# Optimization experiments

Hardware: AMD Instinct MI355X
Metric: run time of the kernel (lower is better)

Reference implementation:

```python
import jax, jax.numpy as jnp
import numpy as np

SEQ, B, IN, H = 2048, 4096, 1, 32


def setup_inputs() -> dict:
    key = jax.random.key(0)
    ks = jax.random.split(key, 8)
    s_ih = 1.0 / np.sqrt(H)  # torch nn.RNN init scale
    return {
        "x": jax.random.normal(ks[0], (SEQ, B, IN), dtype=jnp.float32),
        "hidden": jnp.zeros((1, B, H), dtype=jnp.float32),
        "W_ih": jax.random.uniform(ks[1], (H, IN), jnp.float32, -s_ih, s_ih),
        "b_ih": jax.random.uniform(ks[2], (H,), jnp.float32, -s_ih, s_ih),
        "W_hh": jax.random.uniform(ks[3], (H, H), jnp.float32, -s_ih, s_ih),
        "b_hh": jax.random.uniform(ks[4], (H,), jnp.float32, -s_ih, s_ih),
        "W_fc": jax.random.uniform(ks[5], (IN, H), jnp.float32, -s_ih, s_ih),
        "b_fc": jax.random.uniform(ks[6], (IN,), jnp.float32, -s_ih, s_ih),
    }


def reference(x, hidden, W_ih, b_ih, W_hh, b_hh, W_fc, b_fc):
    # Elman RNN: h_t = tanh(x_t W_ih^T + b_ih + h_{t-1} W_hh^T + b_hh)
    # Precompute the input projection for all timesteps in one GEMM.
    x_proj = jnp.einsum('sbi,hi->sbh', x, W_ih) + b_ih + b_hh  # (SEQ, B, H)
    h0 = hidden[0]  # (B, H), single layer

    def step(h, xp_t):
        h_new = jnp.tanh(xp_t + h @ W_hh.T)
        return h_new, h_new

    _, outputs = jax.lax.scan(step, h0, x_proj)  # outputs: (SEQ, B, H)
    # Trailing Linear: (SEQ, B, H) -> (SEQ, B, IN)
    return jnp.einsum('sbh,oh->sbo', outputs, W_fc) + b_fc
```

## Files before the change

### kernel.cpp

```cpp
#include <hip/hip_runtime.h>

#define SEQ   2048
#define BATCH 4096
#define HD    32

__device__ __forceinline__ float exp2_fast(float a) {
#if __has_builtin(__builtin_amdgcn_exp2f)
    return __builtin_amdgcn_exp2f(a);
#else
    return exp2f(a);
#endif
}

__device__ __forceinline__ float rcp_fast(float a) {
#if __has_builtin(__builtin_amdgcn_rcpf)
    return __builtin_amdgcn_rcpf(a);
#else
    return 1.0f / a;
#endif
}

__device__ __forceinline__ float fast_tanh(float v) {
    float ax = fabsf(v);
    float e  = exp2_fast(ax * -2.8853900817779268f);
    float r  = (1.0f - e) * rcp_fast(1.0f + e);
    return copysignf(r, v);
}

template <int CTRL>
__device__ __forceinline__ float dpp_mov0(float v) {
    return __int_as_float(
        __builtin_amdgcn_update_dpp(0, __float_as_int(v), CTRL, 0xF, 0xF, false));
}

__global__ __launch_bounds__(256) void rnn_elman_kernel(
    const float* __restrict__ x, const float* __restrict__ hidden,
    const float* __restrict__ W_ih, const float* __restrict__ b_ih,
    const float* __restrict__ W_hh, const float* __restrict__ b_hh,
    const float* __restrict__ W_fc, const float* __restrict__ b_fc,
    float* __restrict__ out)
{
    __shared__ float sh[16 * 36];

    const int tid = threadIdx.x;
    const int s   = tid & 15;
    const int eb  = tid >> 4;
    const int e   = blockIdx.x * 16 + eb;
    const int r0  = 2 * s;
    const int r1  = 2 * s + 1;

    float4 w0[8], w1[8];
    {
        const float4* W0 = reinterpret_cast<const float4*>(W_hh + r0 * HD);
        const float4* W1 = reinterpret_cast<const float4*>(W_hh + r1 * HD);
        #pragma unroll
        for (int k = 0; k < 8; ++k) { w0[k] = W0[k]; w1[k] = W1[k]; }
    }
    const float wih0  = W_ih[r0], wih1 = W_ih[r1];
    const float bias0 = b_ih[r0] + b_hh[r0];
    const float bias1 = b_ih[r1] + b_hh[r1];
    const float wfc0  = W_fc[r0], wfc1 = W_fc[r1];
    const float bfc   = b_fc[0];

    float* slot = sh + eb * 36;
    reinterpret_cast<float2*>(slot)[s] =
        make_float2(hidden[e * HD + r0], hidden[e * HD + r1]);
    __builtin_amdgcn_wave_barrier();

    float4 hb[8];
    #pragma unroll
    for (int k = 0; k < 8; ++k) hb[k] = reinterpret_cast<const float4*>(slot)[k];

    float xq0 = x[0 * BATCH + e];
    float xq1 = x[1 * BATCH + e];
    float xq2 = x[2 * BATCH + e];
    float xq3 = x[3 * BATCH + e];

    #pragma unroll 4
    for (int t = 0; t < SEQ; ++t) {
        const float xv = xq0;
        xq0 = xq1; xq1 = xq2; xq2 = xq3;
        {
            int tt = t + 4; tt = tt < SEQ - 1 ? tt : SEQ - 1;
            xq3 = x[tt * BATCH + e];
        }

        float a0a = fmaf(xv, wih0, bias0);
        float a1a = fmaf(xv, wih1, bias1);
        float a0b = 0.f, a0c = 0.f, a0d = 0.f;
        float a1b = 0.f, a1c = 0.f, a1d = 0.f;
        #pragma unroll
        for (int k = 0; k < 8; ++k) {
            const float4 h4 = hb[k];
            const float4 ww = w0[k];
            const float4 vv = w1[k];
            a0a = fmaf(ww.x, h4.x, a0a);
            a0b = fmaf(ww.y, h4.y, a0b);
            a0c = fmaf(ww.z, h4.z, a0c);
            a0d = fmaf(ww.w, h4.w, a0d);
            a1a = fmaf(vv.x, h4.x, a1a);
            a1b = fmaf(vv.y, h4.y, a1b);
            a1c = fmaf(vv.z, h4.z, a1c);
            a1d = fmaf(vv.w, h4.w, a1d);
        }
        const float z0 = (a0a + a0b) + (a0c + a0d);
        const float z1 = (a1a + a1b) + (a1c + a1d);

        const float h0 = fast_tanh(z0);
        const float h1 = fast_tanh(z1);

        reinterpret_cast<float2*>(slot)[s] = make_float2(h0, h1);
        __builtin_amdgcn_wave_barrier();
        #pragma unroll
        for (int k = 0; k < 8; ++k) hb[k] = reinterpret_cast<const float4*>(slot)[k];

        float p = fmaf(h0, wfc0, h1 * wfc1);
        p += dpp_mov0<0x111>(p);
        p += dpp_mov0<0x112>(p);
        p += dpp_mov0<0x114>(p);
        p += dpp_mov0<0x118>(p);
        if (s == 15) out[t * BATCH + e] = p + bfc;
    }
}

extern "C" void kernel_launch(void* const* d_in, const int* in_sizes, int n_in,
                              void* d_out, int out_size, void* d_ws, size_t ws_size,
                              hipStream_t stream) {
    const float* x    = (const float*)d_in[0];
    const float* hid  = (const float*)d_in[1];
    const float* W_ih = (const float*)d_in[2];
    const float* b_ih = (const float*)d_in[3];
    const float* W_hh = (const float*)d_in[4];
    const float* b_hh = (const float*)d_in[5];
    const float* W_fc = (const float*)d_in[6];
    const float* b_fc = (const float*)d_in[7];
    float* out = (float*)d_out;

    dim3 grid(BATCH / 16);
    dim3 block(256);
    rnn_elman_kernel<<<grid, block, 0, stream>>>(x, hid, W_ih, b_ih, W_hh, b_hh,
                                                 W_fc, b_fc, out);
}
```

Before: 594.4 us.

## Split each batch element's hidden matvec across 32 lanes with swizzle exchange

Each batch element now gets 32 lanes instead of 16. Every lane computes half of the K-dimension for its own row and for its partner's row. The partial sums are exchanged with a ds_swizzle xor-16, so each lane produces one hidden unit per step. This halves the per-lane FMA chain and register footprint on the serial recurrence and doubles the thread count, with launch bounds raised to allow more waves. In exchange it adds a cross-lane swizzle and an extra reduction stage on the critical path every timestep.

```diff
diff --git a/kernel.cpp b/kernel.cpp
--- a/kernel.cpp
+++ b/kernel.cpp
@@ -33,43 +33,49 @@
         __builtin_amdgcn_update_dpp(0, __float_as_int(v), CTRL, 0xF, 0xF, false));
 }
 
-__global__ __launch_bounds__(256) void rnn_elman_kernel(
+__device__ __forceinline__ float swz_xor16(float v) {
+    return __int_as_float(__builtin_amdgcn_ds_swizzle(__float_as_int(v), 0x401F));
+}
+
+__global__ __launch_bounds__(256, 2) void rnn_elman_kernel(
     const float* __restrict__ x, const float* __restrict__ hidden,
     const float* __restrict__ W_ih, const float* __restrict__ b_ih,
     const float* __restrict__ W_hh, const float* __restrict__ b_hh,
     const float* __restrict__ W_fc, const float* __restrict__ b_fc,
     float* __restrict__ out)
 {
-    __shared__ float sh[16 * 36];
+    __shared__ float sh[8 * 36];
 
-    const int tid = threadIdx.x;
-    const int s   = tid & 15;
-    const int eb  = tid >> 4;
-    const int e   = blockIdx.x * 16 + eb;
-    const int r0  = 2 * s;
-    const int r1  = 2 * s + 1;
+    const int tid   = threadIdx.x;
+    const int s     = tid & 31;
+    const int half  = s >> 4;
+    const int q     = s & 15;
+    const int eb    = tid >> 5;
+    const int e     = blockIdx.x * 8 + eb;
+    const int r_own = 2 * q + half;
+    const int r_oth = 2 * q + 1 - half;
 
-    float4 w0[8], w1[8];
+    float4 wo[4], wn[4];
     {
-        const float4* W0 = reinterpret_cast<const float4*>(W_hh + r0 * HD);
-        const float4* W1 = reinterpret_cast<const float4*>(W_hh + r1 * HD);
+        const float4* WO = reinterpret_cast<const float4*>(W_hh + r_own * HD + half * 16);
+        const float4* WN = reinterpret_cast<const float4*>(W_hh + r_oth * HD + half * 16);
         #pragma unroll
-        for (int k = 0; k < 8; ++k) { w0[k] = W0[k]; w1[k] = W1[k]; }
+        for (int k = 0; k < 4; ++k) { wo[k] = WO[k]; wn[k] = WN[k]; }
     }
-    const float wih0  = W_ih[r0], wih1 = W_ih[r1];
-    const float bias0 = b_ih[r0] + b_hh[r0];
-    const float bias1 = b_ih[r1] + b_hh[r1];
-    const float wfc0  = W_fc[r0], wfc1 = W_fc[r1];
-    const float bfc   = b_fc[0];
+    const float wih  = W_ih[r_own];
+    const float bias = b_ih[r_own] + b_hh[r_own];
+    const float wfc  = W_fc[r_own];
+    const float bfc  = b_fc[0];
 
     float* slot = sh + eb * 36;
-    reinterpret_cast<float2*>(slot)[s] =
-        make_float2(hidden[e * HD + r0], hidden[e * HD + r1]);
+    const float4* rd = reinterpret_cast<const float4*>(slot + half * 16);
+
+    slot[r_own] = hidden[e * HD + r_own];
     __builtin_amdgcn_wave_barrier();
 
-    float4 hb[8];
+    float4 hb[4];
     #pragma unroll
-    for (int k = 0; k < 8; ++k) hb[k] = reinterpret_cast<const float4*>(slot)[k];
+    for (int k = 0; k < 4; ++k) hb[k] = rd[k];
 
     float xq0 = x[0 * BATCH + e];
     float xq1 = x[1 * BATCH + e];
@@ -85,41 +91,51 @@
             xq3 = x[tt * BATCH + e];
         }
 
-        float a0a = fmaf(xv, wih0, bias0);
-        float a1a = fmaf(xv, wih1, bias1);
-        float a0b = 0.f, a0c = 0.f, a0d = 0.f;
-        float a1b = 0.f, a1c = 0.f, a1d = 0.f;
+        float a0 = fmaf(xv, wih, bias);
+        float a1 = 0.f;
+        float b0 = 0.f, b1 = 0.f;
         #pragma unroll
-        for (int k = 0; k < 8; ++k) {
+        for (int k = 0; k < 2; ++k) {
             const float4 h4 = hb[k];
-            const float4 ww = w0[k];
-            const float4 vv = w1[k];
-            a0a = fmaf(ww.x, h4.x, a0a);
-            a0b = fmaf(ww.y, h4.y, a0b);
-            a0c = fmaf(ww.z, h4.z, a0c);
-            a0d = fmaf(ww.w, h4.w, a0d);
-            a1a = fmaf(vv.x, h4.x, a1a);
-            a1b = fmaf(vv.y, h4.y, a1b);
-            a1c = fmaf(vv.z, h4.z, a1c);
-            a1d = fmaf(vv.w, h4.w, a1d);
+            const float4 h5 = hb[k + 2];
+            const float4 u  = wo[k];
+            const float4 v  = wo[k + 2];
+            const float4 m  = wn[k];
+            const float4 n  = wn[k + 2];
+            a0 = fmaf(u.x, h4.x, a0);
+            a0 = fmaf(u.y, h4.y, a0);
+            a0 = fmaf(u.z, h4.z, a0);
+            a0 = fmaf(u.w, h4.w, a0);
+            a1 = fmaf(v.x, h5.x, a1);
+            a1 = fmaf(v.y, h5.y, a1);
+            a1 = fmaf(v.z, h5.z, a1);
+            a1 = fmaf(v.w, h5.w, a1);
+            b0 = fmaf(m.x, h4.x, b0);
+            b0 = fmaf(m.y, h4.y, b0);
+            b0 = fmaf(m.z, h4.z, b0);
+            b0 = fmaf(m.w, h4.w, b0);
+            b1 = fmaf(n.x, h5.x, b1);
+            b1 = fmaf(n.y, h5.y, b1);
+            b1 = fmaf(n.z, h5.z, b1);
+            b1 = fmaf(n.w, h5.w, b1);
         }
-        const float z0 = (a0a + a0b) + (a0c + a0d);
-        const float z1 = (a1a + a1b) + (a1c + a1d);
+        const float own = a0 + a1;
+        const float oth = b0 + b1;
+        const float z   = own + swz_xor16(oth);
+        const float h   = fast_tanh(z);
 
-        const float h0 = fast_tanh(z0);
-        const float h1 = fast_tanh(z1);
-
-        reinterpret_cast<float2*>(slot)[s] = make_float2(h0, h1);
+        slot[r_own] = h;
         __builtin_amdgcn_wave_barrier();
         #pragma unroll
-        for (int k = 0; k < 8; ++k) hb[k] = reinterpret_cast<const float4*>(slot)[k];
+        for (int k = 0; k < 4; ++k) hb[k] = rd[k];
 
-        float p = fmaf(h0, wfc0, h1 * wfc1);
+        float p = h * wfc;
         p += dpp_mov0<0x111>(p);
         p += dpp_mov0<0x112>(p);
         p += dpp_mov0<0x114>(p);
         p += dpp_mov0<0x118>(p);
-        if (s == 15) out[t * BATCH + e] = p + bfc;
+        p += dpp_mov0<0x142>(p);
+        if (s == 31) out[t * BATCH + e] = p + bfc;
     }
 }
 
@@ -136,7 +152,7 @@
     const float* b_fc = (const float*)d_in[7];
     float* out = (float*)d_out;
 
-    dim3 grid(BATCH / 16);
+    dim3 grid(BATCH / 8);
     dim3 block(256);
     rnn_elman_kernel<<<grid, block, 0, stream>>>(x, hid, W_ih, b_ih, W_hh, b_hh,
                                                  W_fc, b_fc, out);
```

Result: slower. 616.2 us (+3.7%).

## Split hidden dot products across 32 lanes per batch element with DPP reductions

Applied to the files above, without the earlier changes.

Each batch element now gets a full 32 lanes instead of 16. Each lane covers a quarter of the K dimension for four rows, so the recurrent matvec per lane shrinks from 64 to 32 FMAs. Per-step LDS reads drop from eight float4 loads to two. The partial sums are combined with quad-permute DPP moves, and the output projection uses DPP mirrors plus a ds_swizzle xor-16. The grid doubles to 512 blocks and launch bounds request two blocks per CU, trading more waves and extra cross-lane reduction work for a shorter serial dependency chain per timestep.

```diff
diff --git a/kernel.cpp b/kernel.cpp
--- a/kernel.cpp
+++ b/kernel.cpp
@@ -28,98 +28,108 @@
 }
 
 template <int CTRL>
-__device__ __forceinline__ float dpp_mov0(float v) {
+__device__ __forceinline__ float dpp_x(float v) {
     return __int_as_float(
         __builtin_amdgcn_update_dpp(0, __float_as_int(v), CTRL, 0xF, 0xF, false));
 }
 
-__global__ __launch_bounds__(256) void rnn_elman_kernel(
+__device__ __forceinline__ float swz_xor16(float v) {
+    return __int_as_float(__builtin_amdgcn_ds_swizzle(__float_as_int(v), 0x401F));
+}
+
+__global__ __launch_bounds__(256, 2) void rnn_elman_kernel(
     const float* __restrict__ x, const float* __restrict__ hidden,
     const float* __restrict__ W_ih, const float* __restrict__ b_ih,
     const float* __restrict__ W_hh, const float* __restrict__ b_hh,
     const float* __restrict__ W_fc, const float* __restrict__ b_fc,
     float* __restrict__ out)
 {
-    __shared__ float sh[16 * 36];
+    __shared__ float sh[8 * 36];
 
     const int tid = threadIdx.x;
-    const int s   = tid & 15;
-    const int eb  = tid >> 4;
-    const int e   = blockIdx.x * 16 + eb;
-    const int r0  = 2 * s;
-    const int r1  = 2 * s + 1;
+    const int i   = tid & 31;
+    const int ks  = i & 3;
+    const int eb  = tid >> 5;
+    const int e   = blockIdx.x * 8 + eb;
 
-    float4 w0[8], w1[8];
+    float w0[8], w1[8], w2[8], w3[8];
     {
-        const float4* W0 = reinterpret_cast<const float4*>(W_hh + r0 * HD);
-        const float4* W1 = reinterpret_cast<const float4*>(W_hh + r1 * HD);
+        const int rbase = i & ~3;
+        const float* R0 = W_hh + (rbase | (ks ^ 0)) * HD + ks * 8;
+        const float* R1 = W_hh + (rbase | (ks ^ 1)) * HD + ks * 8;
+        const float* R2 = W_hh + (rbase | (ks ^ 2)) * HD + ks * 8;
+        const float* R3 = W_hh + (rbase | (ks ^ 3)) * HD + ks * 8;
         #pragma unroll
-        for (int k = 0; k < 8; ++k) { w0[k] = W0[k]; w1[k] = W1[k]; }
+        for (int m = 0; m < 8; ++m) {
+            w0[m] = R0[m]; w1[m] = R1[m]; w2[m] = R2[m]; w3[m] = R3[m];
+        }
     }
-    const float wih0  = W_ih[r0], wih1 = W_ih[r1];
-    const float bias0 = b_ih[r0] + b_hh[r0];
-    const float bias1 = b_ih[r1] + b_hh[r1];
-    const float wfc0  = W_fc[r0], wfc1 = W_fc[r1];
-    const float bfc   = b_fc[0];
+    const float wih  = W_ih[i];
+    const float bias = b_ih[i] + b_hh[i];
+    const float wfc  = W_fc[i];
+    const float bfc  = b_fc[0];
 
     float* slot = sh + eb * 36;
-    reinterpret_cast<float2*>(slot)[s] =
-        make_float2(hidden[e * HD + r0], hidden[e * HD + r1]);
+    const float4* rd = reinterpret_cast<const float4*>(slot + ks * 8);
+
+    slot[i] = hidden[e * HD + i];
     __builtin_amdgcn_wave_barrier();
+    float4 hb0 = rd[0], hb1 = rd[1];
 
-    float4 hb[8];
-    #pragma unroll
-    for (int k = 0; k < 8; ++k) hb[k] = reinterpret_cast<const float4*>(slot)[k];
-
-    float xq0 = x[0 * BATCH + e];
-    float xq1 = x[1 * BATCH + e];
-    float xq2 = x[2 * BATCH + e];
-    float xq3 = x[3 * BATCH + e];
+    float xq0 = x[(size_t)0 * BATCH + e];
+    float xq1 = x[(size_t)1 * BATCH + e];
+    float xq2 = x[(size_t)2 * BATCH + e];
+    float xq3 = x[(size_t)3 * BATCH + e];
 
     #pragma unroll 4
     for (int t = 0; t < SEQ; ++t) {
         const float xv = xq0;
         xq0 = xq1; xq1 = xq2; xq2 = xq3;
         {
-            int tt = t + 4; tt = tt < SEQ - 1 ? tt : SEQ - 1;
-            xq3 = x[tt * BATCH + e];
+            int tt = t + 4; tt = tt < SEQ ? tt : SEQ - 1;
+            const float* xr = x + (size_t)tt * BATCH;
+            xq3 = xr[e];
         }
 
-        float a0a = fmaf(xv, wih0, bias0);
-        float a1a = fmaf(xv, wih1, bias1);
-        float a0b = 0.f, a0c = 0.f, a0d = 0.f;
-        float a1b = 0.f, a1c = 0.f, a1d = 0.f;
-        #pragma unroll
-        for (int k = 0; k < 8; ++k) {
-            const float4 h4 = hb[k];
-            const float4 ww = w0[k];
-            const float4 vv = w1[k];
-            a0a = fmaf(ww.x, h4.x, a0a);
-            a0b = fmaf(ww.y, h4.y, a0b);
-            a0c = fmaf(ww.z, h4.z, a0c);
-            a0d = fmaf(ww.w, h4.w, a0d);
-            a1a = fmaf(vv.x, h4.x, a1a);
-            a1b = fmaf(vv.y, h4.y, a1b);
-            a1c = fmaf(vv.z, h4.z, a1c);
-            a1d = fmaf(vv.w, h4.w, a1d);
+        float p0 = fmaf(xv, wih, bias);
+        float p1 = 0.f, p2 = 0.f, p3 = 0.f;
+        {
+            const float* hv0 = reinterpret_cast<const float*>(&hb0);
+            const float* hv1 = reinterpret_cast<const float*>(&hb1);
+            #pragma unroll
+            for (int m = 0; m < 4; ++m) {
+                const float ha = hv0[m];
+                const float hc = hv1[m];
+                p0 = fmaf(w0[m], ha, p0);
+                p1 = fmaf(w1[m], ha, p1);
+                p2 = fmaf(w2[m], ha, p2);
+                p3 = fmaf(w3[m], ha, p3);
+                p0 = fmaf(w0[m + 4], hc, p0);
+                p1 = fmaf(w1[m + 4], hc, p1);
+                p2 = fmaf(w2[m + 4], hc, p2);
+                p3 = fmaf(w3[m + 4], hc, p3);
+            }
         }
-        const float z0 = (a0a + a0b) + (a0c + a0d);
-        const float z1 = (a1a + a1b) + (a1c + a1d);
 
-        const float h0 = fast_tanh(z0);
-        const float h1 = fast_tanh(z1);
+        const float q0 = p0 + dpp_x<0xB1>(p1);
+        const float q1 = p2 + dpp_x<0xB1>(p3);
+        const float z  = q0 + dpp_x<0x4E>(q1);
+        const float h  = fast_tanh(z);
 
-        reinterpret_cast<float2*>(slot)[s] = make_float2(h0, h1);
+        slot[i] = h;
         __builtin_amdgcn_wave_barrier();
-        #pragma unroll
-        for (int k = 0; k < 8; ++k) hb[k] = reinterpret_cast<const float4*>(slot)[k];
+        hb0 = rd[0]; hb1 = rd[1];
 
-        float p = fmaf(h0, wfc0, h1 * wfc1);
-        p += dpp_mov0<0x111>(p);
-        p += dpp_mov0<0x112>(p);
-        p += dpp_mov0<0x114>(p);
-        p += dpp_mov0<0x118>(p);
-        if (s == 15) out[t * BATCH + e] = p + bfc;
+        float u = h * wfc;
+        u += dpp_x<0xB1>(u);
+        u += dpp_x<0x4E>(u);
+        u += dpp_x<0x141>(u);
+        u += dpp_x<0x140>(u);
+        u += swz_xor16(u);
+        if ((tid & 31) == 0) {
+            float* orow = out + (size_t)t * BATCH;
+            orow[e] = u + bfc;
+        }
     }
 }
 
@@ -136,7 +146,7 @@
     const float* b_fc = (const float*)d_in[7];
     float* out = (float*)d_out;
 
-    dim3 grid(BATCH / 16);
+    dim3 grid(BATCH / 8);
     dim3 block(256);
     rnn_elman_kernel<<<grid, block, 0, stream>>>(x, hid, W_ih, b_ih, W_hh, b_hh,
                                                  W_fc, b_fc, out);
```

Result: slower. 609.4 us (+2.5%).
